# Kernel tuning notes

Hardware: AMD Instinct MI355X
Metric: run time of the kernel (lower is better)

## Reference

```python
import jax, jax.numpy as jnp
import numpy as np

N_NODES = 100000
N_EDGES = 1600000
F_IN, HID, N_CLS = 128, 128, 64


def setup_inputs() -> dict:
    key = jax.random.key(0)
    ks = jax.random.split(key, 9)
    x = jax.random.normal(ks[0], (N_NODES, F_IN), dtype=jnp.float32)
    edge_index = jax.random.randint(ks[1], (2, N_EDGES), 0, N_NODES, dtype=jnp.int64)
    edge_attr = jax.random.uniform(ks[2], (N_EDGES,), dtype=jnp.float32)
    def glorot(k, fi, fo):
        lim = (6.0 / (fi + fo)) ** 0.5
        return jax.random.uniform(k, (fi, fo), minval=-lim, maxval=lim, dtype=jnp.float32)
    return {
        "x": x, "edge_index": edge_index, "edge_attr": edge_attr,
        "W1": glorot(ks[3], F_IN, HID), "b1": jnp.zeros((HID,), jnp.float32),
        "W2": glorot(ks[4], HID, HID), "b2": jnp.zeros((HID,), jnp.float32),
        "W3": glorot(ks[5], HID, N_CLS), "b3": jnp.zeros((N_CLS,), jnp.float32),
    }


def reference(x, edge_index, edge_attr, W1, b1, W2, b2, W3, b3):
    N = x.shape[0]
    # PyG GCNConv: add self-loops with weight 1, symmetric normalization
    loop = jnp.arange(N, dtype=edge_index.dtype)
    src = jnp.concatenate([edge_index[0], loop])  # [E+N]
    dst = jnp.concatenate([edge_index[1], loop])
    w = jnp.concatenate([edge_attr, jnp.ones((N,), edge_attr.dtype)])
    deg = jax.ops.segment_sum(w, dst, num_segments=N)  # [N]
    dinv = jnp.where(deg > 0, deg ** -0.5, 0.0)
    norm = dinv[src] * w * dinv[dst]  # [E+N]

    def gcn_conv(h, W, b):
        h = h @ W                                 # [N, out]
        msg = norm[:, None] * h[src]              # [E+N, out] gather
        agg = jax.ops.segment_sum(msg, dst, num_segments=N)  # scatter-add
        return agg + b

    # dropout is identity in eval mode
    h = jax.nn.relu(gcn_conv(x, W1, b1))
    h = jax.nn.relu(gcn_conv(h, W2, b2))
    return gcn_conv(h, W3, b3)
```

## Files before the change

### kernel.cpp

```cpp
#include <hip/hip_runtime.h>
#include <hip/hip_fp16.h>


#define F_IN 128
#define HID  128
#define N_CLS 64

#define EDGE_CHUNK 8192
#define BCAP 6144

typedef _Float16 h8 __attribute__((ext_vector_type(8)));
typedef float f32x4 __attribute__((ext_vector_type(4)));


template <int BN, typename TA, bool CVTW>
__device__ __forceinline__
void mm_body(const TA* __restrict__ A, const float* __restrict__ Wsrc,
             const _Float16* __restrict__ WT, __half* __restrict__ C,
             int nrows, int bid, char* smem) {
    constexpr int K   = 128;
    constexpr int NCT = BN / 16;
    constexpr int KP  = K + 8;
    constexpr int CP  = BN + 8;
    _Float16* lw = (_Float16*)smem;
    _Float16* lc = (_Float16*)(smem + (size_t)BN * KP * 2);
    const int tid  = threadIdx.x;
    const int wave = tid >> 6;
    const int lane = tid & 63;
    const int bm0  = bid * 64;

    if constexpr (CVTW) {
        for (int c = tid; c < BN * K; c += 256) {
            int n = c & (BN - 1);
            int k = c / BN;
            lw[n * KP + k] = (_Float16)Wsrc[k * BN + n];
        }
    } else {
        for (int c = tid; c < BN * 16; c += 256) {
            int n = c >> 4, k = (c & 15) * 8;
            *(h8*)&lw[n * KP + k] = *(const h8*)&WT[n * 128 + k];
        }
    }
    __syncthreads();

    f32x4 acc[NCT];
#pragma unroll
    for (int ct = 0; ct < NCT; ++ct)
#pragma unroll
        for (int i = 0; i < 4; ++i) acc[ct][i] = 0.0f;

    const int row = bm0 + wave * 16 + (lane & 15);
    const int kb  = (lane >> 4) * 8;
    const bool rok = row < nrows;

#pragma unroll
    for (int kk = 0; kk < 4; ++kk) {
        const int k0 = kk * 32 + kb;
        h8 va;
        if (rok) {
            if constexpr (__is_same(TA, float)) {
                float4 f0 = *(const float4*)&A[(size_t)row * K + k0];
                float4 f1 = *(const float4*)&A[(size_t)row * K + k0 + 4];
                va[0] = (_Float16)f0.x; va[1] = (_Float16)f0.y;
                va[2] = (_Float16)f0.z; va[3] = (_Float16)f0.w;
                va[4] = (_Float16)f1.x; va[5] = (_Float16)f1.y;
                va[6] = (_Float16)f1.z; va[7] = (_Float16)f1.w;
            } else {
                va = *(const h8*)&A[(size_t)row * K + k0];
            }
        } else {
#pragma unroll
            for (int i = 0; i < 8; ++i) va[i] = (_Float16)0.0f;
        }
#pragma unroll
        for (int ct = 0; ct < NCT; ++ct) {
            h8 vb = *(const h8*)&lw[(ct * 16 + (lane & 15)) * KP + k0];
            acc[ct] = __builtin_amdgcn_mfma_f32_16x16x32_f16(va, vb, acc[ct], 0, 0, 0);
        }
    }

#pragma unroll
    for (int ct = 0; ct < NCT; ++ct)
#pragma unroll
        for (int r = 0; r < 4; ++r)
            lc[(wave * 16 + (lane >> 4) * 4 + r) * CP + ct * 16 + (lane & 15)] =
                (_Float16)acc[ct][r];
    __syncthreads();

    constexpr int NCH = (64 * BN / 8) / 256;
#pragma unroll
    for (int i = 0; i < NCH; ++i) {
        int c = i * 256 + tid;
        int r = c / (BN / 8), col = (c % (BN / 8)) * 8;
        int grow = bm0 + r;
        if (grow < nrows)
            *(h8*)&C[(size_t)grow * BN + col] = *(const h8*)&lc[r * CP + col];
    }
}


__device__ __forceinline__
void bscatter_body(const int* __restrict__ src, const int* __restrict__ dst,
                   const float* __restrict__ w, int* __restrict__ cursor,
                   int2* __restrict__ stage, int E, int bid, char* smem) {
    int* lcnt  = (int*)smem;
    int* lbase = (int*)(smem + 2048);
    const int t = threadIdx.x;
    for (int i = t; i < 512; i += 256) lcnt[i] = 0;
    __syncthreads();
    const int base = bid * EDGE_CHUNK;
    int d[32];
#pragma unroll
    for (int i = 0; i < 32; ++i) {
        int e = base + i * 256 + t;
        d[i] = (e < E) ? dst[e] : -1;
        if (d[i] >= 0) atomicAdd(&lcnt[d[i] >> 8], 1);
    }
    __syncthreads();
    for (int i = t; i < 512; i += 256) {
        int c = lcnt[i];
        lbase[i] = (c > 0) ? atomicAdd(&cursor[i], c) : 0;
        lcnt[i] = 0;
    }
    __syncthreads();
#pragma unroll
    for (int i = 0; i < 32; ++i) {
        int e = base + i * 256 + t;
        if (e >= E) continue;
        int dd = d[i];
        int b  = dd >> 8;
        int p  = lbase[b] + atomicAdd(&lcnt[b], 1);
        if (p < BCAP)
            stage[(size_t)b * BCAP + p] =
                make_int2(src[e] | ((dd & 255) << 20), __float_as_int(w[e]));
    }
}


#define SMEM_FRONT ((HID * (128 + 8) + 64 * (HID + 8)) * 2)

__launch_bounds__(256)
__global__ void k_front(const int* __restrict__ src, const int* __restrict__ dst,
                        const float* __restrict__ w, int* __restrict__ cursor,
                        int2* __restrict__ stage, int E,
                        const float* __restrict__ x, const float* __restrict__ W1,
                        __half* __restrict__ bufH, int nrows, int nEB) {
    __shared__ __align__(16) char smem[SMEM_FRONT];
    if ((int)blockIdx.x < nEB)
        bscatter_body(src, dst, w, cursor, stage, E, blockIdx.x, smem);
    else
        mm_body<HID, float, true>(x, W1, nullptr, bufH, nrows, blockIdx.x - nEB, smem);
}


__global__ void k_slabdeg(const int2* __restrict__ stage, const int* __restrict__ cursor,
                          float* __restrict__ dinv, int* __restrict__ bbase,
                          int n, int NB, int E) {
    __shared__ float degf[256];
    __shared__ int   sh[512];
    const int b = blockIdx.x, t = threadIdx.x;
    if (t < 256) degf[t] = 0.0f;
    __syncthreads();
    const int cnt0 = cursor[b];
    const int cnt  = (cnt0 < BCAP) ? cnt0 : BCAP;
    const int2* sl = stage + (size_t)b * BCAP;
    for (int j = t; j < cnt; j += 512) {
        int2 s = sl[j];
        atomicAdd(&degf[s.x >> 20], __int_as_float(s.y));
    }
    __syncthreads();
    const int node = b * 256 + t;
    if (t < 256 && node < n) dinv[node] = rsqrtf(1.0f + degf[t]);

    if (b == 0) {
        sh[t] = (t < NB) ? min(cursor[t], BCAP) : 0;
        __syncthreads();
        for (int off = 1; off < 512; off <<= 1) {
            int x2 = (t >= off) ? sh[t - off] : 0;
            __syncthreads();
            sh[t] += x2;
            __syncthreads();
        }
        if (t < NB) bbase[t] = (t == 0) ? 0 : sh[t - 1];
        if (t == 0) bbase[NB] = E;
    }
}


__launch_bounds__(256)
__global__ void k_csrw(const int2* __restrict__ stage, const int* __restrict__ bbase,
                       const float* __restrict__ dinv,
                       int* __restrict__ row_ptr, int2* __restrict__ csr,
                       int n, int E,
                       const float* __restrict__ W2, const float* __restrict__ W3,
                       _Float16* __restrict__ W2T, _Float16* __restrict__ W3T, int NB) {
    __shared__ int scn[256];
    __shared__ int cur[256];
    const int t = threadIdx.x;
    if ((int)blockIdx.x >= NB) {
        int id = ((int)blockIdx.x - NB) * 256 + t;
        if (id < 16384) {
            int n2 = id >> 7, k = id & 127;
            W2T[n2 * 128 + k] = (_Float16)W2[k * 128 + n2];
        } else {
            int i = id - 16384;
            int n3 = i >> 7, k = i & 127;
            W3T[n3 * 128 + k] = (_Float16)W3[k * 64 + n3];
        }
        return;
    }
    const int b = blockIdx.x;
    const int beg = bbase[b];
    const int cnt = bbase[b + 1] - beg;
    const int2* sl = stage + (size_t)b * BCAP;
    scn[t] = 0;
    __syncthreads();
    for (int j = t; j < cnt; j += 256)
        atomicAdd(&scn[sl[j].x >> 20], 1);
    __syncthreads();
    int own = scn[t];
    __syncthreads();
    for (int off = 1; off < 256; off <<= 1) {
        int x2 = (t >= off) ? scn[t - off] : 0;
        __syncthreads();
        scn[t] += x2;
        __syncthreads();
    }
    const int excl = scn[t] - own;
    const int node = b * 256 + t;
    if (node < n) row_ptr[node] = beg + excl;
    cur[t] = excl;
    __syncthreads();
    for (int j = t; j < cnt; j += 256) {
        int2 s = sl[j];
        int dlow  = s.x >> 20;
        int srcid = s.x & 0xFFFFF;
        float nw  = dinv[srcid] * __int_as_float(s.y);
        int pos = beg + atomicAdd(&cur[dlow], 1);
        csr[pos] = make_int2(srcid, __float_as_int(nw));
    }
    if (b == 0 && t == 0) row_ptr[n] = E;
}


template <int BN, typename TA>
__launch_bounds__(256)
__global__ void k_mm_mfma(const TA* __restrict__ A, const _Float16* __restrict__ WT,
                          __half* __restrict__ C, int nrows) {
    __shared__ __align__(16) char smem[(BN * (128 + 8) + 64 * (BN + 8)) * 2];
    mm_body<BN, TA, false>(A, nullptr, WT, C, nrows, blockIdx.x, smem);
}


template <int NCOL, bool RELU, typename TO>
__launch_bounds__(256)
__global__ void k_agg(const __half* __restrict__ XW, const int* __restrict__ row_ptr,
                      const int2* __restrict__ csr,
                      const float* __restrict__ dinv, const float* __restrict__ bias,
                      TO* __restrict__ out, int n) {
    constexpr int PER = NCOL / 64;
    int wid  = (blockIdx.x * blockDim.x + threadIdx.x) >> 6;
    int lane = threadIdx.x & 63;
    if (wid >= n) return;
    const int node = __builtin_amdgcn_readfirstlane(wid);
    const float dn  = dinv[node];
    const int  beg  = row_ptr[node];
    const int  end  = row_ptr[node + 1];

    float a0, a1 = 0.0f;
    {
        if (PER == 2) {
            __half2 hv = *(const __half2*)&XW[(size_t)node * NCOL + lane * 2];
            a0 = dn * __low2float(hv); a1 = dn * __high2float(hv);
        } else {
            a0 = dn * __half2float(XW[(size_t)node * NCOL + lane]);
        }
    }

    int j = beg;
    for (; j + 4 <= end; j += 4) {
        int2 e0 = csr[j + 0], e1 = csr[j + 1], e2 = csr[j + 2], e3 = csr[j + 3];
        float w0 = __int_as_float(e0.y), w1 = __int_as_float(e1.y);
        float w2 = __int_as_float(e2.y), w3 = __int_as_float(e3.y);
        if (PER == 2) {
            __half2 v0 = *(const __half2*)&XW[(size_t)e0.x * NCOL + lane * 2];
            __half2 v1 = *(const __half2*)&XW[(size_t)e1.x * NCOL + lane * 2];
            __half2 v2 = *(const __half2*)&XW[(size_t)e2.x * NCOL + lane * 2];
            __half2 v3 = *(const __half2*)&XW[(size_t)e3.x * NCOL + lane * 2];
            a0 = fmaf(w0, __low2float(v0), a0); a1 = fmaf(w0, __high2float(v0), a1);
            a0 = fmaf(w1, __low2float(v1), a0); a1 = fmaf(w1, __high2float(v1), a1);
            a0 = fmaf(w2, __low2float(v2), a0); a1 = fmaf(w2, __high2float(v2), a1);
            a0 = fmaf(w3, __low2float(v3), a0); a1 = fmaf(w3, __high2float(v3), a1);
        } else {
            float v0 = __half2float(XW[(size_t)e0.x * NCOL + lane]);
            float v1 = __half2float(XW[(size_t)e1.x * NCOL + lane]);
            float v2 = __half2float(XW[(size_t)e2.x * NCOL + lane]);
            float v3 = __half2float(XW[(size_t)e3.x * NCOL + lane]);
            a0 = fmaf(w0, v0, a0);
            a0 = fmaf(w1, v1, a0);
            a0 = fmaf(w2, v2, a0);
            a0 = fmaf(w3, v3, a0);
        }
    }
    for (; j < end; ++j) {
        int2 e = csr[j];
        float nw = __int_as_float(e.y);
        if (PER == 2) {
            __half2 v = *(const __half2*)&XW[(size_t)e.x * NCOL + lane * 2];
            a0 = fmaf(nw, __low2float(v), a0); a1 = fmaf(nw, __high2float(v), a1);
        } else {
            a0 = fmaf(nw, __half2float(XW[(size_t)e.x * NCOL + lane]), a0);
        }
    }

    if (PER == 2) {
        a0 = fmaf(dn, a0, bias[lane * 2 + 0]);
        a1 = fmaf(dn, a1, bias[lane * 2 + 1]);
        if (RELU) { a0 = fmaxf(a0, 0.0f); a1 = fmaxf(a1, 0.0f); }
        if constexpr (__is_same(TO, float)) {
            *(float2*)&out[(size_t)node * NCOL + lane * 2] = make_float2(a0, a1);
        } else {
            *(__half2*)&out[(size_t)node * NCOL + lane * 2] = __floats2half2_rn(a0, a1);
        }
    } else {
        a0 = fmaf(dn, a0, bias[lane]);
        if (RELU) a0 = fmaxf(a0, 0.0f);
        if constexpr (__is_same(TO, float)) {
            out[(size_t)node * NCOL + lane] = a0;
        } else {
            out[(size_t)node * NCOL + lane] = __float2half(a0);
        }
    }
}


extern "C" void kernel_launch(void* const* d_in, const int* in_sizes, int n_in,
                              void* d_out, int out_size, void* d_ws, size_t ws_size,
                              hipStream_t stream) {
    const float* x  = (const float*)d_in[0];
    const int*   ei = (const int*)d_in[1];
    const float* ea = (const float*)d_in[2];
    const float* W1 = (const float*)d_in[3];
    const float* b1 = (const float*)d_in[4];
    const float* W2 = (const float*)d_in[5];
    const float* b2 = (const float*)d_in[6];
    const float* W3 = (const float*)d_in[7];
    const float* b3 = (const float*)d_in[8];

    const int N = in_sizes[0] / F_IN;
    const int E = in_sizes[1] / 2;
    const int* src = ei;
    const int* dst = ei + E;
    const int NB = (N + 255) / 256;

    char* ws = (char*)d_ws;
    size_t off = 0;
    auto alloc = [&](size_t bytes) -> void* {
        void* p = ws + off;
        off += (bytes + 255) & ~(size_t)255;
        return p;
    };
    __half*    bufH    = (__half*)   alloc((size_t)N * HID * sizeof(__half));
    __half*    bufH2   = (__half*)   alloc((size_t)N * HID * sizeof(__half));
    float*     dinv    = (float*)    alloc((size_t)N * sizeof(float));
    int*       row_ptr = (int*)      alloc((size_t)(N + 1) * sizeof(int));
    int2*      csr     = (int2*)     alloc((size_t)E * sizeof(int2));
    int2*      stage   = (int2*)     alloc((size_t)NB * BCAP * sizeof(int2));
    int*       cursor  = (int*)      alloc((size_t)NB * sizeof(int));
    int*       bbase   = (int*)      alloc((size_t)(NB + 1) * sizeof(int));
    _Float16*  W2T     = (_Float16*) alloc((size_t)128 * 128 * sizeof(_Float16));
    _Float16*  W3T     = (_Float16*) alloc((size_t)64 * 128 * sizeof(_Float16));
    (void)ws_size;

    const int BLK = 256;
    const int nEB = (E + EDGE_CHUNK - 1) / EDGE_CHUNK;
    const int gMM = (N + 63) / 64;

    hipMemsetAsync(cursor, 0, (size_t)NB * sizeof(int), stream);
    k_front<<<nEB + gMM, BLK, 0, stream>>>(src, dst, ea, cursor, stage, E,
                                           x, W1, bufH, N, nEB);
    k_slabdeg<<<NB, 512, 0, stream>>>(stage, cursor, dinv, bbase, N, NB, E);
    k_csrw<<<NB + 96, BLK, 0, stream>>>(stage, bbase, dinv, row_ptr, csr, N, E,
                                        W2, W3, W2T, W3T, NB);

    const int gAG = (N + 3) / 4;

    k_agg<HID, true, __half><<<gAG, BLK, 0, stream>>>(bufH, row_ptr, csr, dinv, b1, bufH2, N);
    k_mm_mfma<HID, __half><<<gMM, BLK, 0, stream>>>(bufH2, W2T, bufH, N);
    k_agg<HID, true, __half><<<gAG, BLK, 0, stream>>>(bufH, row_ptr, csr, dinv, b2, bufH2, N);
    k_mm_mfma<N_CLS, __half><<<gMM, BLK, 0, stream>>>(bufH2, W3T, bufH, N);
    k_agg<N_CLS, false, float><<<gAG, BLK, 0, stream>>>(bufH, row_ptr, csr, dinv, b3, (float*)d_out, N);
}
```

Baseline: 280.4 us.

## Store hidden features in column-sliced layout and aggregate per 16-column slice

The 128-wide hidden feature matrices are now stored as eight 16-column slices (slice-major, node, 16 halves), written by the matmul epilogues and read by the next matmul. A new aggregation kernel gives each block a single slice, so every gathered row is 32 bytes and a slice's working set (about 3.2 MB) can stay cache-resident across neighbour gathers. Within a wave, eight sub-groups split a node's edges and the partial sums are combined with cross-lane shuffles. The cost is eight times more blocks, each rereading the CSR indices and weights, plus 32-byte gather granularity and a shuffle reduction.

```diff
diff --git a/kernel.cpp b/kernel.cpp
--- a/kernel.cpp
+++ b/kernel.cpp
@@ -13,7 +13,7 @@
 typedef float f32x4 __attribute__((ext_vector_type(4)));
 
 
-template <int BN, typename TA, bool CVTW>
+template <int BN, typename TA, bool CVTW, bool ASLICE, bool CSLICE>
 __device__ __forceinline__
 void mm_body(const TA* __restrict__ A, const float* __restrict__ Wsrc,
              const _Float16* __restrict__ WT, __half* __restrict__ C,
@@ -65,6 +65,8 @@
                 va[2] = (_Float16)f0.z; va[3] = (_Float16)f0.w;
                 va[4] = (_Float16)f1.x; va[5] = (_Float16)f1.y;
                 va[6] = (_Float16)f1.z; va[7] = (_Float16)f1.w;
+            } else if constexpr (ASLICE) {
+                va = *(const h8*)&A[((size_t)(k0 >> 4) * nrows + row) * 16 + (k0 & 15)];
             } else {
                 va = *(const h8*)&A[(size_t)row * K + k0];
             }
@@ -93,8 +95,14 @@
         int c = i * 256 + tid;
         int r = c / (BN / 8), col = (c % (BN / 8)) * 8;
         int grow = bm0 + r;
-        if (grow < nrows)
-            *(h8*)&C[(size_t)grow * BN + col] = *(const h8*)&lc[r * CP + col];
+        if (grow < nrows) {
+            if constexpr (CSLICE) {
+                *(h8*)&C[((size_t)(col >> 4) * nrows + grow) * 16 + (col & 15)] =
+                    *(const h8*)&lc[r * CP + col];
+            } else {
+                *(h8*)&C[(size_t)grow * BN + col] = *(const h8*)&lc[r * CP + col];
+            }
+        }
     }
 }
 
@@ -144,12 +152,13 @@
                         const float* __restrict__ w, int* __restrict__ cursor,
                         int2* __restrict__ stage, int E,
                         const float* __restrict__ x, const float* __restrict__ W1,
-                        __half* __restrict__ bufH, int nrows, int nEB) {
+                        __half* __restrict__ bufS, int nrows, int nEB) {
     __shared__ __align__(16) char smem[SMEM_FRONT];
     if ((int)blockIdx.x < nEB)
         bscatter_body(src, dst, w, cursor, stage, E, blockIdx.x, smem);
     else
-        mm_body<HID, float, true>(x, W1, nullptr, bufH, nrows, blockIdx.x - nEB, smem);
+        mm_body<HID, float, true, false, true>(x, W1, nullptr, bufS, nrows,
+                                               blockIdx.x - nEB, smem);
 }
 
 
@@ -243,22 +252,66 @@
 }
 
 
-template <int BN, typename TA>
+template <int BN, bool CSLICE>
 __launch_bounds__(256)
-__global__ void k_mm_mfma(const TA* __restrict__ A, const _Float16* __restrict__ WT,
+__global__ void k_mm_mfma(const _Float16* __restrict__ A, const _Float16* __restrict__ WT,
                           __half* __restrict__ C, int nrows) {
     __shared__ __align__(16) char smem[(BN * (128 + 8) + 64 * (BN + 8)) * 2];
-    mm_body<BN, TA, false>(A, nullptr, WT, C, nrows, blockIdx.x, smem);
-}
-
-
-template <int NCOL, bool RELU, typename TO>
+    mm_body<BN, _Float16, false, true, CSLICE>(A, nullptr, WT, C, nrows,
+                                               blockIdx.x, smem);
+}
+
+
+template <bool RELU>
+__launch_bounds__(256)
+__global__ void k_agg_s(const __half* __restrict__ T, const int* __restrict__ row_ptr,
+                        const int2* __restrict__ csr, const float* __restrict__ dinv,
+                        const float* __restrict__ bias, __half* __restrict__ out,
+                        int n, int N) {
+    const int slice = blockIdx.x & 7;
+    const int grp   = blockIdx.x >> 3;
+    int node = grp * 4 + (threadIdx.x >> 6);
+    if (node >= n) return;
+    node = __builtin_amdgcn_readfirstlane(node);
+    const int lane = threadIdx.x & 63;
+    const int sub  = lane >> 3;
+    const int c2   = lane & 7;
+    const float dn = dinv[node];
+    const int beg = row_ptr[node];
+    const int total = row_ptr[node + 1] - beg + 1;
+    const __half* tb = T + (size_t)slice * N * 16;
+
+    float a0 = 0.0f, a1 = 0.0f;
+    for (int i = sub; i < total; i += 8) {
+        int sidx; float w;
+        if (i == 0) { sidx = node; w = dn; }
+        else { int2 e = csr[beg + i - 1]; sidx = e.x; w = __int_as_float(e.y); }
+        __half2 v = *(const __half2*)&tb[(size_t)sidx * 16 + c2 * 2];
+        a0 = fmaf(w, __low2float(v), a0);
+        a1 = fmaf(w, __high2float(v), a1);
+    }
+#pragma unroll
+    for (int m = 8; m <= 32; m <<= 1) {
+        a0 += __shfl_xor(a0, m, 64);
+        a1 += __shfl_xor(a1, m, 64);
+    }
+    if (sub == 0) {
+        float2 bb = *(const float2*)&bias[slice * 16 + c2 * 2];
+        a0 = fmaf(dn, a0, bb.x);
+        a1 = fmaf(dn, a1, bb.y);
+        if (RELU) { a0 = fmaxf(a0, 0.0f); a1 = fmaxf(a1, 0.0f); }
+        *(__half2*)&out[((size_t)slice * N + node) * 16 + c2 * 2] =
+            __floats2half2_rn(a0, a1);
+    }
+}
+
+
+template <int NCOL, bool RELU>
 __launch_bounds__(256)
 __global__ void k_agg(const __half* __restrict__ XW, const int* __restrict__ row_ptr,
                       const int2* __restrict__ csr,
                       const float* __restrict__ dinv, const float* __restrict__ bias,
-                      TO* __restrict__ out, int n) {
-    constexpr int PER = NCOL / 64;
+                      float* __restrict__ out, int n) {
     int wid  = (blockIdx.x * blockDim.x + threadIdx.x) >> 6;
     int lane = threadIdx.x & 63;
     if (wid >= n) return;
@@ -267,70 +320,31 @@
     const int  beg  = row_ptr[node];
     const int  end  = row_ptr[node + 1];
 
-    float a0, a1 = 0.0f;
-    {
-        if (PER == 2) {
-            __half2 hv = *(const __half2*)&XW[(size_t)node * NCOL + lane * 2];
-            a0 = dn * __low2float(hv); a1 = dn * __high2float(hv);
-        } else {
-            a0 = dn * __half2float(XW[(size_t)node * NCOL + lane]);
-        }
-    }
+    float a0 = dn * __half2float(XW[(size_t)node * NCOL + lane]);
 
     int j = beg;
     for (; j + 4 <= end; j += 4) {
         int2 e0 = csr[j + 0], e1 = csr[j + 1], e2 = csr[j + 2], e3 = csr[j + 3];
         float w0 = __int_as_float(e0.y), w1 = __int_as_float(e1.y);
         float w2 = __int_as_float(e2.y), w3 = __int_as_float(e3.y);
-        if (PER == 2) {
-            __half2 v0 = *(const __half2*)&XW[(size_t)e0.x * NCOL + lane * 2];
-            __half2 v1 = *(const __half2*)&XW[(size_t)e1.x * NCOL + lane * 2];
-            __half2 v2 = *(const __half2*)&XW[(size_t)e2.x * NCOL + lane * 2];
-            __half2 v3 = *(const __half2*)&XW[(size_t)e3.x * NCOL + lane * 2];
-            a0 = fmaf(w0, __low2float(v0), a0); a1 = fmaf(w0, __high2float(v0), a1);
-            a0 = fmaf(w1, __low2float(v1), a0); a1 = fmaf(w1, __high2float(v1), a1);
-            a0 = fmaf(w2, __low2float(v2), a0); a1 = fmaf(w2, __high2float(v2), a1);
-            a0 = fmaf(w3, __low2float(v3), a0); a1 = fmaf(w3, __high2float(v3), a1);
-        } else {
-            float v0 = __half2float(XW[(size_t)e0.x * NCOL + lane]);
-            float v1 = __half2float(XW[(size_t)e1.x * NCOL + lane]);
-            float v2 = __half2float(XW[(size_t)e2.x * NCOL + lane]);
-            float v3 = __half2float(XW[(size_t)e3.x * NCOL + lane]);
-            a0 = fmaf(w0, v0, a0);
-            a0 = fmaf(w1, v1, a0);
-            a0 = fmaf(w2, v2, a0);
-            a0 = fmaf(w3, v3, a0);
-        }
+        float v0 = __half2float(XW[(size_t)e0.x * NCOL + lane]);
+        float v1 = __half2float(XW[(size_t)e1.x * NCOL + lane]);
+        float v2 = __half2float(XW[(size_t)e2.x * NCOL + lane]);
+        float v3 = __half2float(XW[(size_t)e3.x * NCOL + lane]);
+        a0 = fmaf(w0, v0, a0);
+        a0 = fmaf(w1, v1, a0);
+        a0 = fmaf(w2, v2, a0);
+        a0 = fmaf(w3, v3, a0);
     }
     for (; j < end; ++j) {
         int2 e = csr[j];
-        float nw = __int_as_float(e.y);
-        if (PER == 2) {
-            __half2 v = *(const __half2*)&XW[(size_t)e.x * NCOL + lane * 2];
-            a0 = fmaf(nw, __low2float(v), a0); a1 = fmaf(nw, __high2float(v), a1);
-        } else {
-            a0 = fmaf(nw, __half2float(XW[(size_t)e.x * NCOL + lane]), a0);
-        }
-    }
-
-    if (PER == 2) {
-        a0 = fmaf(dn, a0, bias[lane * 2 + 0]);
-        a1 = fmaf(dn, a1, bias[lane * 2 + 1]);
-        if (RELU) { a0 = fmaxf(a0, 0.0f); a1 = fmaxf(a1, 0.0f); }
-        if constexpr (__is_same(TO, float)) {
-            *(float2*)&out[(size_t)node * NCOL + lane * 2] = make_float2(a0, a1);
-        } else {
-            *(__half2*)&out[(size_t)node * NCOL + lane * 2] = __floats2half2_rn(a0, a1);
-        }
-    } else {
-        a0 = fmaf(dn, a0, bias[lane]);
-        if (RELU) a0 = fmaxf(a0, 0.0f);
-        if constexpr (__is_same(TO, float)) {
-            out[(size_t)node * NCOL + lane] = a0;
-        } else {
-            out[(size_t)node * NCOL + lane] = __float2half(a0);
-        }
-    }
+        a0 = fmaf(__int_as_float(e.y),
+                  __half2float(XW[(size_t)e.x * NCOL + lane]), a0);
+    }
+
+    a0 = fmaf(dn, a0, bias[lane]);
+    if (RELU) a0 = fmaxf(a0, 0.0f);
+    out[(size_t)node * NCOL + lane] = a0;
 }
 
 
@@ -360,8 +374,8 @@
         off += (bytes + 255) & ~(size_t)255;
         return p;
     };
-    __half*    bufH    = (__half*)   alloc((size_t)N * HID * sizeof(__half));
-    __half*    bufH2   = (__half*)   alloc((size_t)N * HID * sizeof(__half));
+    __half*    bufS1   = (__half*)   alloc((size_t)N * HID * sizeof(__half));
+    __half*    bufS2   = (__half*)   alloc((size_t)N * HID * sizeof(__half));
     float*     dinv    = (float*)    alloc((size_t)N * sizeof(float));
     int*       row_ptr = (int*)      alloc((size_t)(N + 1) * sizeof(int));
     int2*      csr     = (int2*)     alloc((size_t)E * sizeof(int2));
@@ -370,6 +384,7 @@
     int*       bbase   = (int*)      alloc((size_t)(NB + 1) * sizeof(int));
     _Float16*  W2T     = (_Float16*) alloc((size_t)128 * 128 * sizeof(_Float16));
     _Float16*  W3T     = (_Float16*) alloc((size_t)64 * 128 * sizeof(_Float16));
+    __half*    bufH3   = bufS1;
     (void)ws_size;
 
     const int BLK = 256;
@@ -378,16 +393,18 @@
 
     hipMemsetAsync(cursor, 0, (size_t)NB * sizeof(int), stream);
     k_front<<<nEB + gMM, BLK, 0, stream>>>(src, dst, ea, cursor, stage, E,
-                                           x, W1, bufH, N, nEB);
+                                           x, W1, bufS1, N, nEB);
     k_slabdeg<<<NB, 512, 0, stream>>>(stage, cursor, dinv, bbase, N, NB, E);
     k_csrw<<<NB + 96, BLK, 0, stream>>>(stage, bbase, dinv, row_ptr, csr, N, E,
                                         W2, W3, W2T, W3T, NB);
 
-    const int gAG = (N + 3) / 4;
-
-    k_agg<HID, true, __half><<<gAG, BLK, 0, stream>>>(bufH, row_ptr, csr, dinv, b1, bufH2, N);
-    k_mm_mfma<HID, __half><<<gMM, BLK, 0, stream>>>(bufH2, W2T, bufH, N);
-    k_agg<HID, true, __half><<<gAG, BLK, 0, stream>>>(bufH, row_ptr, csr, dinv, b2, bufH2, N);
-    k_mm_mfma<N_CLS, __half><<<gMM, BLK, 0, stream>>>(bufH2, W3T, bufH, N);
-    k_agg<N_CLS, false, float><<<gAG, BLK, 0, stream>>>(bufH, row_ptr, csr, dinv, b3, (float*)d_out, N);
-}
+    const int gAGS = 8 * ((N + 3) / 4);
+    const int gAG3 = (N + 3) / 4;
+
+    k_agg_s<true><<<gAGS, BLK, 0, stream>>>(bufS1, row_ptr, csr, dinv, b1, bufS2, N, N);
+    k_mm_mfma<HID, true><<<gMM, BLK, 0, stream>>>((const _Float16*)bufS2, W2T, bufS1, N);
+    k_agg_s<true><<<gAGS, BLK, 0, stream>>>(bufS1, row_ptr, csr, dinv, b2, bufS2, N, N);
+    k_mm_mfma<N_CLS, false><<<gMM, BLK, 0, stream>>>((const _Float16*)bufS2, W3T, bufH3, N);
+    k_agg<N_CLS, false><<<gAG3, BLK, 0, stream>>>(bufH3, row_ptr, csr, dinv, b3,
+                                                  (float*)d_out, N);
+}
```

After: 633.7 us. +126.0%, slower.
